# Kernel tuning notes

Hardware: AMD Instinct MI355X
Metric: run time of the kernel (lower is better)

The kernel has to match this reference:

```python
import jax, jax.numpy as jnp
from jax import lax
import numpy as np

DN = ('NCHW', 'OIHW', 'NCHW')

def conv2d_same(x, w, b):
    # 5x5, stride 1, pad 2 == SAME
    y = lax.conv_general_dilated(x, w, (1, 1), 'SAME', dimension_numbers=DN)
    return y + b[None, :, None, None]

def setup_inputs() -> dict:
    key = jax.random.key(0)
    ks = jax.random.split(key, 5)
    B, S, D = 8, 2048, 1024
    k55 = 0.2  # ~1/sqrt(25) init scale
    return {
        'x':  jax.random.normal(ks[0], (B, S, D), dtype=jnp.float32),
        'w1': jax.random.normal(ks[1], (1, 1, 5, 5), dtype=jnp.float32) * k55,
        'b1': jnp.zeros((1,), jnp.float32),
        'w2': jax.random.normal(ks[2], (1, 1, 5, 5), dtype=jnp.float32) * k55,
        'b2': jnp.zeros((1,), jnp.float32),
        'w3': jax.random.normal(ks[3], (1, 2, 5, 5), dtype=jnp.float32) * k55,
        'b3': jnp.zeros((1,), jnp.float32),
        'w4': jax.random.normal(ks[4], (1, 1, 5, 5), dtype=jnp.float32) * k55,
        'b4': jnp.zeros((1,), jnp.float32),
    }

def reference(x, w1, b1, w2, b2, w3, b3, w4, b4):
    # x: [b, s, d]
    xT = jnp.swapaxes(x, 1, 2)                              # [b, d, s]
    # self-similarity, softmax over BATCH dim (dim=0, as in original)
    NSSM = jax.nn.softmax(jnp.einsum('bsd,btd->bst', x, x), axis=0)   # [b, s, s]
    conv_x  = conv2d_same(x[:, None],  w1, b1)[:, 0]        # [b, s, d]
    conv_xT = conv2d_same(xT[:, None], w2, b2)[:, 0]        # [b, d, s]
    Attention_map = jax.nn.softmax(jnp.matmul(conv_x, conv_xT), axis=0)  # [b, s, s]
    Moca_map = conv2d_same(jnp.stack([NSSM, Attention_map], axis=1), w3, b3)[:, 0]  # [b, s, s]
    conv_g = conv2d_same(x[:, None], w4, b4)[:, 0]          # [b, s, d]
    Wz = jnp.matmul(Moca_map, conv_g)                       # [b, s, d]
    return Wz + x
```

## Files before the change

### kernel.cpp

```cpp
#include <hip/hip_runtime.h>

#define Bz 8
#define Sz 2048
#define Dz 1024

typedef __attribute__((ext_vector_type(8))) _Float16 f16x8;
typedef __attribute__((ext_vector_type(8))) short short8v;
typedef __attribute__((ext_vector_type(4))) short short4v;
typedef __attribute__((ext_vector_type(4))) float f32x4;

__device__ __forceinline__ short f2h(float f) {
    _Float16 h = (_Float16)f;
    return __builtin_bit_cast(short, h);
}
__device__ __forceinline__ float h2f(short s) {
    return (float)__builtin_bit_cast(_Float16, s);
}
__device__ __forceinline__ void gld16(const void* g, void* l) {
    __builtin_amdgcn_global_load_lds(
        (const __attribute__((address_space(1))) void*)g,
        (__attribute__((address_space(3))) void*)l, 16, 0, 0);
}

__global__ __launch_bounds__(256) void conv3_kernel(
    const float* __restrict__ x,
    const float* __restrict__ w1, const float* __restrict__ b1,
    const float* __restrict__ w2, const float* __restrict__ b2,
    short* __restrict__ x16, short* __restrict__ C1f, short* __restrict__ C2f)
{
    __shared__ float w[50];
    __shared__ float bias[2];
    const size_t SD = (size_t)Sz * Dz;
    int tid = threadIdx.x;
    if (tid < 25) w[tid] = w1[tid];
    else if (tid < 50) w[tid] = w2[tid - 25];
    if (tid == 50) { bias[0] = b1[0]; bias[1] = b2[0]; }
    __syncthreads();

    int d4 = tid * 4;
    int y = blockIdx.y;
    int s = ((y & 7) << 8) | (y >> 3);
    int b = blockIdx.z;
    const float* xb = x + (size_t)b * SD + d4;

    float wv[5][12];
#pragma unroll
    for (int i = 0; i < 5; i++) {
        int ss = s + i - 2;
        int ssc = ss < 0 ? 0 : (ss >= Sz ? Sz - 1 : ss);
        const float* rp = xb + (size_t)ssc * Dz;
        if (d4 > 0) *(float4*)&wv[i][0] = *(const float4*)(rp - 4);
        else { wv[i][0] = wv[i][1] = wv[i][2] = wv[i][3] = 0.f; }
        *(float4*)&wv[i][4] = *(const float4*)rp;
        if (d4 < 1020) *(float4*)&wv[i][8] = *(const float4*)(rp + 4);
        else { wv[i][8] = wv[i][9] = wv[i][10] = wv[i][11] = 0.f; }
        if (ss != ssc) {
#pragma unroll
            for (int q = 0; q < 12; q++) wv[i][q] = 0.f;
        }
    }

    float o1[4] = {}, o2[4] = {};
#pragma unroll
    for (int i = 0; i < 5; i++)
#pragma unroll
        for (int j = 0; j < 5; j++) {
            float c1w = w[i * 5 + j], c2w = w[25 + j * 5 + i];
#pragma unroll
            for (int q = 0; q < 4; q++) {
                float v = wv[i][q + j + 2];
                o1[q] = fmaf(c1w, v, o1[q]);
                o2[q] = fmaf(c2w, v, o2[q]);
            }
        }
    size_t o = (size_t)b * SD + (size_t)s * Dz + d4;
    short4v hx, h1, h2;
#pragma unroll
    for (int q = 0; q < 4; q++) {
        hx[q] = f2h(wv[2][q + 4]);
        h1[q] = f2h(o1[q] + bias[0]);
        h2[q] = f2h(o2[q] + bias[1]);
    }
    *(short4v*)(x16 + o) = hx;
    *(short4v*)(C1f + o) = h1;
    *(short4v*)(C2f + o) = h2;
}

__global__ __launch_bounds__(256) void convT_kernel(
    const float* __restrict__ x, const float* __restrict__ w4,
    const float* __restrict__ b4, short* __restrict__ C4T)
{
    __shared__ float xs[68][73];
    __shared__ short ct[64][72];
    __shared__ float w[25];
    __shared__ float bb;
    const size_t SD = (size_t)Sz * Dz;
    int tid = threadIdx.x;
    if (tid < 25) w[tid] = w4[tid];
    if (tid == 25) bb = b4[0];

    int s0 = blockIdx.x * 64, d0 = blockIdx.y * 64, b = blockIdx.z;
    const float* xb = x + (size_t)b * SD;
    for (int k = tid; k < 68 * 68; k += 256) {
        int r = k / 68, c = k - r * 68;
        int gr = s0 - 2 + r, gc = d0 - 2 + c;
        float v = 0.f;
        if (gr >= 0 && gr < Sz && gc >= 0 && gc < Dz) v = xb[(size_t)gr * Dz + gc];
        xs[r][c] = v;
    }
    __syncthreads();

    int sl = tid & 63, dg = tid >> 6;
    float acc[16];
#pragma unroll
    for (int q = 0; q < 16; q++) acc[q] = bb;
#pragma unroll
    for (int i = 0; i < 5; i++) {
        float row[20];
#pragma unroll
        for (int m = 0; m < 20; m++) row[m] = xs[sl + i][dg * 16 + m];
#pragma unroll
        for (int j = 0; j < 5; j++) {
            float wv = w[i * 5 + j];
#pragma unroll
            for (int q = 0; q < 16; q++) acc[q] = fmaf(wv, row[q + j], acc[q]);
        }
    }
#pragma unroll
    for (int q = 0; q < 16; q++) ct[dg * 16 + q][sl] = f2h(acc[q]);
    __syncthreads();

    int dl = tid >> 2, sc = (tid & 3) * 16;
    f16x8 v0 = *(const f16x8*)&ct[dl][sc];
    f16x8 v1 = *(const f16x8*)&ct[dl][sc + 8];
    short* op = C4T + (size_t)b * SD + (size_t)(d0 + dl) * Sz + s0 + sc;
    *(f16x8*)op = v0;
    *(f16x8*)(op + 8) = v1;
}

__global__ __launch_bounds__(512) void logit_f16(
    const short* __restrict__ Ag, const short* __restrict__ Bg,
    const short* __restrict__ Aa, const short* __restrict__ Ba,
    short* __restrict__ Qg, short* __restrict__ Qa,
    int rlo, int sqoff, long PS)
{
    __shared__ short sA[3][4096];
    __shared__ short sB[3][4096];

    int flat = blockIdx.x + 16 * (blockIdx.y + 8 * blockIdx.z);
    int nid = (flat & 7) * 256 + (flat >> 3);
    int bx = nid & 15;
    int by = (nid >> 4) & 7;
    int bz = nid >> 7;

    const int map = bz >> 3, bzb = bz & 7;
    if (map == 0) {
        int nt = bx - sqoff;
        if (nt >= 0 && nt < 8 && nt < by) return;
    }

    const size_t SD = (size_t)Sz * Dz;
    const int K = Dz;
    const short* A = (map ? Aa : Ag) + (size_t)bzb * SD;
    const short* B = (map ? Ba : Bg) + (size_t)bzb * SD;
    short* Q = (map ? Qa : Qg) + (size_t)bzb * PS;

    const int m0 = by * 128, n0 = bx * 128;
    const int t = threadIdx.x;
    const int lane = t & 63;
    const int w = t >> 6;
    const int wm = w >> 2, wn = w & 3;
    const int fr = lane & 15;
    const int kb = lane >> 4;

    const int s_  = (t & 7) ^ ((t >> 3) & 7);
    const int h_  = s_ >> 2, kbs = s_ & 3;
    const int lrow = t >> 3;
    const int rowAs = m0 + lrow + h_ * 64;
    const int rowBs = n0 + lrow + h_ * 64;
    const size_t aOff = (size_t)rowAs * K * 2 + kbs * 16;
    const size_t bOff = (size_t)rowBs * K * 2 + kbs * 16;

    int rdA[4], rdB[2];
#pragma unroll
    for (int f = 0; f < 4; f++) {
        int row = wm * 64 + f * 16 + fr;
        rdA[f] = (row & 63) * 128 + ((((row >> 6) * 4 + kb) ^ (fr & 7)) * 16);
    }
#pragma unroll
    for (int g = 0; g < 2; g++) {
        int row = wn * 32 + g * 16 + fr;
        rdB[g] = (row & 63) * 128 + ((((row >> 6) * 4 + kb) ^ (fr & 7)) * 16);
    }

    f32x4 acc[4][2];
#pragma unroll
    for (int i = 0; i < 4; i++)
#pragma unroll
        for (int j = 0; j < 2; j++) acc[i][j] = (f32x4){0.f, 0.f, 0.f, 0.f};

    auto STAGE = [&](int buf, int k0) {
        gld16((const char*)A + aOff + (size_t)k0 * 2, (char*)&sA[buf][0] + t * 16);
        gld16((const char*)B + bOff + (size_t)k0 * 2, (char*)&sB[buf][0] + t * 16);
    };
    auto COMPUTE = [&](int buf) {
        const char* pA = (const char*)&sA[buf][0];
        const char* pB = (const char*)&sB[buf][0];
        f16x8 af[4], bfr[2];
#pragma unroll
        for (int f = 0; f < 4; f++) af[f] = *(const f16x8*)(pA + rdA[f]);
#pragma unroll
        for (int g = 0; g < 2; g++) bfr[g] = *(const f16x8*)(pB + rdB[g]);
#pragma unroll
        for (int mf = 0; mf < 4; mf++)
#pragma unroll
            for (int nf = 0; nf < 2; nf++)
                acc[mf][nf] = __builtin_amdgcn_mfma_f32_16x16x32_f16(af[mf], bfr[nf], acc[mf][nf], 0, 0, 0);
    };

    const int niter = K / 32;
    STAGE(0, 0);
    STAGE(1, 32);
    int cs = 0, ss = 2;
    for (int it = 0; it < niter; ++it) {
        if (it < niter - 1) { asm volatile("s_waitcnt vmcnt(2)" ::: "memory"); }
        else                { asm volatile("s_waitcnt vmcnt(0)" ::: "memory"); }
        __builtin_amdgcn_sched_barrier(0);
        __builtin_amdgcn_s_barrier();
        if (it + 2 < niter) STAGE(ss, (it + 2) * 32);
        COMPUTE(cs);
        cs = cs == 2 ? 0 : cs + 1;
        ss = ss == 2 ? 0 : ss + 1;
    }

#pragma unroll
    for (int mf = 0; mf < 4; mf++)
#pragma unroll
        for (int nf = 0; nf < 2; nf++) {
            int col = n0 + wn * 32 + nf * 16 + fr;
#pragma unroll
            for (int r = 0; r < 4; r++) {
                int rowg = m0 + wm * 64 + mf * 16 + kb * 4 + r;
                float o = acc[mf][nf][r];
                if (map == 0 && rlo + rowg == col) o -= 1024.f;
                Q[(size_t)rowg * Sz + col] = f2h(o);
            }
        }
}

__global__ __launch_bounds__(256) void mirror_g(
    short* __restrict__ F, int o0, long PS)
{
    __shared__ short ts[128][136];
    int p = blockIdx.x, b = blockIdx.y;
    int mi = 1, base = 0;
    while (p >= base + mi) { base += mi; mi++; }
    int nt = p - base;
    short* Fb = F + (size_t)b * PS;
    int t = threadIdx.x;
    int rr = t >> 1, c0 = (t & 1) * 64;
    const short* src = Fb + (size_t)(nt * 128 + rr) * Sz + o0 + mi * 128 + c0;
#pragma unroll
    for (int j = 0; j < 8; j++)
        *(short8v*)&ts[rr][c0 + j * 8] = *(const short8v*)(src + j * 8);
    __syncthreads();
    short* dst = Fb + (size_t)(mi * 128 + rr) * Sz + o0 + nt * 128 + c0;
#pragma unroll
    for (int j = 0; j < 8; j++) {
        short8v v;
#pragma unroll
        for (int e = 0; e < 8; e++) v[e] = ts[c0 + j * 8 + e][rr];
        *(short8v*)(dst + j * 8) = v;
    }
}

__global__ __launch_bounds__(256) void softmax_ip(
    short* __restrict__ Qg, short* __restrict__ Qa, int nElem, long ps)
{
    int i8 = (blockIdx.x * 256 + threadIdx.x) * 8;
    if (i8 >= nElem) return;
    short* Q = blockIdx.z ? Qa : Qg;

    short8v v[Bz];
    float f[Bz][8];
#pragma unroll
    for (int b = 0; b < Bz; b++) {
        v[b] = *(const short8v*)(Q + i8 + (size_t)b * ps);
#pragma unroll
        for (int e = 0; e < 8; e++) f[b][e] = h2f(v[b][e]);
    }
#pragma unroll
    for (int e = 0; e < 8; e++) {
        float mx = f[0][e];
#pragma unroll
        for (int b = 1; b < Bz; b++) mx = fmaxf(mx, f[b][e]);
        float sum = 0.f;
#pragma unroll
        for (int b = 0; b < Bz; b++) { f[b][e] = __expf(f[b][e] - mx); sum += f[b][e]; }
        float inv = 1.f / sum;
#pragma unroll
        for (int b = 0; b < Bz; b++) v[b][e] = f2h(f[b][e] * inv);
    }
#pragma unroll
    for (int b = 0; b < Bz; b++)
        *(short8v*)(Q + i8 + (size_t)b * ps) = v[b];
}

__global__ __launch_bounds__(256) void slab_copy(
    const short* __restrict__ Fg, const short* __restrict__ Fa,
    short* __restrict__ slab, long PS)
{
    int idx = blockIdx.x * 256 + threadIdx.x;
    int e = idx * 8;
    int map = e >> 16;
    int rem = e & 65535;
    int b = rem >> 13;
    int rem2 = rem & 8191;
    int row = rem2 >> 11;
    int col = rem2 & 2047;
    const short* src = (map ? Fa : Fg) + (size_t)b * PS + (size_t)(1020 + row) * Sz + col;
    *(short8v*)(slab + e) = *(const short8v*)src;
}

__global__ __launch_bounds__(256) void moca_kernel(
    const short* __restrict__ Gs, const short* __restrict__ As,
    const short* __restrict__ slab,
    const float* __restrict__ w3, const float* __restrict__ b3,
    short* __restrict__ Mout,
    int o0, int rlo, int slabLo, long psIn, long psOut)
{
    __shared__ float w[50];
    __shared__ float bb;
    int tid = threadIdx.x;
    if (tid < 50) w[tid] = w3[tid];
    if (tid == 50) bb = b3[0];
    __syncthreads();

    int t8 = tid * 8;
    int so = blockIdx.y, b = blockIdx.z;
    int s = o0 + so;
    const short* Gp = Gs + (size_t)b * psIn;
    const short* Ap = As + (size_t)b * psIn;

    float acc[8];
#pragma unroll
    for (int q = 0; q < 8; q++) acc[q] = bb;

#pragma unroll
    for (int i = 0; i < 5; i++) {
        int sr = s + i - 2;
        if (sr < 0 || sr >= Sz) continue;
        const short *gp, *ap;
        size_t ro;
        if (sr >= rlo) { gp = Gp; ap = Ap; ro = (size_t)(sr - rlo) * Sz; }
        else {
            gp = slab + (size_t)b * 8192;
            ap = slab + 65536 + (size_t)b * 8192;
            ro = (size_t)(sr - slabLo) * Sz;
        }
        float gw[16], aw[16];
#pragma unroll
        for (int g = 0; g < 4; g++) {
            int c0 = t8 - 4 + g * 4;
            if (c0 >= 0 && c0 + 3 < Sz) {
                short4v gv = *(const short4v*)(gp + ro + c0);
                short4v av = *(const short4v*)(ap + ro + c0);
#pragma unroll
                for (int e = 0; e < 4; e++) { gw[g * 4 + e] = h2f(gv[e]); aw[g * 4 + e] = h2f(av[e]); }
            } else {
#pragma unroll
                for (int e = 0; e < 4; e++) { gw[g * 4 + e] = 0.f; aw[g * 4 + e] = 0.f; }
            }
        }
#pragma unroll
        for (int j = 0; j < 5; j++) {
            float wg = w[i * 5 + j], wa = w[25 + i * 5 + j];
#pragma unroll
            for (int q = 0; q < 8; q++)
                acc[q] = fmaf(wg, gw[q + j + 2], fmaf(wa, aw[q + j + 2], acc[q]));
        }
    }
    short4v r0, r1;
#pragma unroll
    for (int q = 0; q < 4; q++) { r0[q] = f2h(acc[q]); r1[q] = f2h(acc[q + 4]); }
    short* op = Mout + (size_t)b * psOut + (size_t)so * Sz + t8;
    *(short4v*)op = r0;
    *(short4v*)(op + 4) = r1;
}

__global__ __launch_bounds__(512) void gemm_wz(
    const short* __restrict__ A, const short* __restrict__ B,
    const float* __restrict__ Src, float* __restrict__ C,
    int M, long sAb)
{
    __shared__ short sA[3][4096];
    __shared__ short sB[3][4096];

    int gx = gridDim.x, gy = gridDim.y;
    int total = gx * gy * gridDim.z;
    int flat = blockIdx.x + gx * (blockIdx.y + gy * blockIdx.z);
    int cpx = total >> 3;
    int nid = (flat & 7) * cpx + (flat >> 3);
    int bx = nid % gx;
    int tmp = nid / gx;
    int by = tmp % gy;
    int bz = tmp / gy;

    const size_t SD = (size_t)Sz * Dz;
    const int K = Sz;
    A += (size_t)bz * sAb;
    B += (size_t)bz * SD;
    Src += (size_t)bz * SD;
    C += (size_t)bz * SD;

    const int m0 = by * 128, n0 = bx * 128;
    const int t = threadIdx.x;
    const int lane = t & 63;
    const int w = t >> 6;
    const int wm = w >> 2, wn = w & 3;
    const int fr = lane & 15;
    const int kb = lane >> 4;

    const int s_  = (t & 7) ^ ((t >> 3) & 7);
    const int h_  = s_ >> 2, kbs = s_ & 3;
    const int lrow = t >> 3;
    int rowAs = m0 + lrow + h_ * 64; if (rowAs > M - 1) rowAs = M - 1;
    const int rowBs = n0 + lrow + h_ * 64;
    const size_t aOff = (size_t)rowAs * K * 2 + kbs * 16;
    const size_t bOff = (size_t)rowBs * K * 2 + kbs * 16;

    int rdA[4], rdB[2];
#pragma unroll
    for (int f = 0; f < 4; f++) {
        int row = wm * 64 + f * 16 + fr;
        rdA[f] = (row & 63) * 128 + ((((row >> 6) * 4 + kb) ^ (fr & 7)) * 16);
    }
#pragma unroll
    for (int g = 0; g < 2; g++) {
        int row = wn * 32 + g * 16 + fr;
        rdB[g] = (row & 63) * 128 + ((((row >> 6) * 4 + kb) ^ (fr & 7)) * 16);
    }

    f32x4 acc[4][2];
#pragma unroll
    for (int i = 0; i < 4; i++)
#pragma unroll
        for (int j = 0; j < 2; j++) acc[i][j] = (f32x4){0.f, 0.f, 0.f, 0.f};

    auto STAGE = [&](int buf, int k0) {
        gld16((const char*)A + aOff + (size_t)k0 * 2, (char*)&sA[buf][0] + t * 16);
        gld16((const char*)B + bOff + (size_t)k0 * 2, (char*)&sB[buf][0] + t * 16);
    };
    auto COMPUTE = [&](int buf) {
        const char* pA = (const char*)&sA[buf][0];
        const char* pB = (const char*)&sB[buf][0];
        f16x8 af[4], bfr[2];
#pragma unroll
        for (int f = 0; f < 4; f++) af[f] = *(const f16x8*)(pA + rdA[f]);
#pragma unroll
        for (int g = 0; g < 2; g++) bfr[g] = *(const f16x8*)(pB + rdB[g]);
#pragma unroll
        for (int mf = 0; mf < 4; mf++)
#pragma unroll
            for (int nf = 0; nf < 2; nf++)
                acc[mf][nf] = __builtin_amdgcn_mfma_f32_16x16x32_f16(af[mf], bfr[nf], acc[mf][nf], 0, 0, 0);
    };

    const int niter = K / 32;
    STAGE(0, 0);
    STAGE(1, 32);
    int cs = 0, ss = 2;
    for (int it = 0; it < niter; ++it) {
        if (it < niter - 1) { asm volatile("s_waitcnt vmcnt(2)" ::: "memory"); }
        else                { asm volatile("s_waitcnt vmcnt(0)" ::: "memory"); }
        __builtin_amdgcn_sched_barrier(0);
        __builtin_amdgcn_s_barrier();
        if (it + 2 < niter) STAGE(ss, (it + 2) * 32);
        COMPUTE(cs);
        cs = cs == 2 ? 0 : cs + 1;
        ss = ss == 2 ? 0 : ss + 1;
    }

#pragma unroll
    for (int mf = 0; mf < 4; mf++)
#pragma unroll
        for (int nf = 0; nf < 2; nf++) {
            int col = n0 + wn * 32 + nf * 16 + fr;
#pragma unroll
            for (int r = 0; r < 4; r++) {
                int rowg = m0 + wm * 64 + mf * 16 + kb * 4 + r;
                if (rowg < M)
                    C[(size_t)rowg * Dz + col] = acc[mf][nf][r] + Src[(size_t)rowg * Dz + col];
            }
        }
}

extern "C" void kernel_launch(void* const* d_in, const int* in_sizes, int n_in,
                              void* d_out, int out_size, void* d_ws, size_t ws_size,
                              hipStream_t stream)
{
    const float* x  = (const float*)d_in[0];
    const float* w1 = (const float*)d_in[1];
    const float* b1 = (const float*)d_in[2];
    const float* w2 = (const float*)d_in[3];
    const float* b2 = (const float*)d_in[4];
    const float* w3 = (const float*)d_in[5];
    const float* b3 = (const float*)d_in[6];
    const float* w4 = (const float*)d_in[7];
    const float* b4 = (const float*)d_in[8];
    float* out = (float*)d_out;

    const size_t SD = (size_t)Sz * Dz;
    const size_t BSD2 = (size_t)Bz * SD * 2;

    char* ws = (char*)d_ws;
    short* x16 = (short*)(ws);
    short* C1f = (short*)(ws + 1 * BSD2);
    short* C2f = (short*)(ws + 2 * BSD2);
    short* C4T = (short*)(ws + 3 * BSD2);
    char* strip0 = ws + 4 * BSD2;

    const size_t PS  = (size_t)1024 * Sz;
    const size_t PSM = (size_t)1026 * Sz;
    short* Fg   = (short*)strip0;
    short* Fa   = Fg + (size_t)Bz * PS;
    short* Mf   = Fa + (size_t)Bz * PS;
    short* slab = Mf + (size_t)Bz * PSM;

    conv3_kernel<<<dim3(1, Sz, Bz), 256, 0, stream>>>(
        x, w1, b1, w2, b2, x16, C1f, C2f);
    convT_kernel<<<dim3(Sz / 64, Dz / 64, Bz), 256, 0, stream>>>(x, w4, b4, C4T);

    const int ne = 1024 * Sz;

    logit_f16<<<dim3(16, 8, 16), 512, 0, stream>>>(
        x16, x16, C1f, C2f, Fg, Fa, 0, 0, (long)PS);
    mirror_g<<<dim3(28, Bz), 256, 0, stream>>>(Fg, 0, (long)PS);
    softmax_ip<<<dim3((ne / 8 + 255) / 256, 1, 2), 256, 0, stream>>>(Fg, Fa, ne, (long)PS);
    slab_copy<<<dim3(64), 256, 0, stream>>>(Fg, Fa, slab, (long)PS);
    moca_kernel<<<dim3(1, 1022, Bz), 256, 0, stream>>>(
        Fg, Fa, slab, w3, b3, Mf, 0, 0, 0, (long)PS, (long)PSM);
    gemm_wz<<<dim3(Dz / 128, 8, Bz), 512, 0, stream>>>(
        Mf, C4T, x, out, 1022, (long)PSM);

    logit_f16<<<dim3(16, 8, 16), 512, 0, stream>>>(
        x16 + (size_t)1024 * Dz, x16, C1f + (size_t)1024 * Dz, C2f,
        Fg, Fa, 1024, 8, (long)PS);
    mirror_g<<<dim3(28, Bz), 256, 0, stream>>>(Fg, 1024, (long)PS);
    softmax_ip<<<dim3((ne / 8 + 255) / 256, 1, 2), 256, 0, stream>>>(Fg, Fa, ne, (long)PS);
    moca_kernel<<<dim3(1, 1026, Bz), 256, 0, stream>>>(
        Fg, Fa, slab, w3, b3, Mf, 1022, 1024, 1020, (long)PS, (long)PSM);
    gemm_wz<<<dim3(Dz / 128, 9, Bz), 512, 0, stream>>>(
        Mf, C4T, x + (size_t)1022 * Dz, out + (size_t)1022 * Dz, 1026, (long)PSM);
}
```

Measured before the change: 628.8 us.

## Enlarge logit GEMM tiles to 256x256 with a double-buffered quarter-step MFMA schedule

Replaces the 128x128 logit GEMM with a 256x256-tile kernel. It uses a 128KB LDS double buffer over 64-wide K tiles and issues MFMAs in four quadrant phases per K half. Loads are interleaved with barriers and vmcnt waits, and s_setprio raises priority around the MFMA bursts. The goal is higher arithmetic intensity and less global/LDS traffic per FLOP in the dominant logit matmuls. The cost is coarser symmetry skipping at 256-tile granularity, so some redundant diagonal work is done, and only one block fits per CU.

```diff
diff --git a/kernel.cpp b/kernel.cpp
--- a/kernel.cpp
+++ b/kernel.cpp
@@ -138,25 +138,21 @@
     *(f16x8*)(op + 8) = v1;
 }
 
-__global__ __launch_bounds__(512) void logit_f16(
+__global__ __launch_bounds__(512, 2) void logit8_f16(
     const short* __restrict__ Ag, const short* __restrict__ Bg,
     const short* __restrict__ Aa, const short* __restrict__ Ba,
     short* __restrict__ Qg, short* __restrict__ Qa,
-    int rlo, int sqoff, long PS)
-{
-    __shared__ short sA[3][4096];
-    __shared__ short sB[3][4096];
-
-    int flat = blockIdx.x + 16 * (blockIdx.y + 8 * blockIdx.z);
-    int nid = (flat & 7) * 256 + (flat >> 3);
-    int bx = nid & 15;
-    int by = (nid >> 4) & 7;
-    int bz = nid >> 7;
-
+    int rlo, int sq256off, long PS)
+{
+    __shared__ char lds[131072];
+
+    int flat = blockIdx.x + 8 * (blockIdx.y + 4 * blockIdx.z);
+    int nid = (flat & 7) * 64 + (flat >> 3);
+    int bx = nid & 7, by = (nid >> 3) & 3, bz = nid >> 5;
     const int map = bz >> 3, bzb = bz & 7;
     if (map == 0) {
-        int nt = bx - sqoff;
-        if (nt >= 0 && nt < 8 && nt < by) return;
+        int ntl = bx - sq256off;
+        if (ntl >= 0 && ntl < 4 && ntl < by) return;
     }
 
     const size_t SD = (size_t)Sz * Dz;
@@ -164,6 +160,310 @@
     const short* A = (map ? Aa : Ag) + (size_t)bzb * SD;
     const short* B = (map ? Ba : Bg) + (size_t)bzb * SD;
     short* Q = (map ? Qa : Qg) + (size_t)bzb * PS;
+
+    const int m0 = by * 256, n0 = bx * 256;
+    const int t = threadIdx.x;
+    const int lane = t & 63;
+    const int w = t >> 6;
+    const int wm = w >> 2, wn = w & 3;
+    const int fr = lane & 15;
+    const int kb = lane >> 4;
+
+    const int cc16 = ((t & 7) ^ ((t >> 3) & 7)) * 16;
+    const int tr = t >> 3;
+    const int bdst = (t >> 8) * 8192 + ((t >> 3) & 31) * 128 + (t & 7) * 16;
+
+    auto STA = [&](int tile, int h) {
+        char* base = lds + (tile & 1) * 65536;
+#pragma unroll
+        for (int j = 0; j < 2; j++) {
+            int row = m0 + j * 128 + h * 64 + tr;
+            gld16((const char*)A + ((size_t)row * K + tile * 64) * 2 + cc16,
+                  base + j * 16384 + h * 8192 + t * 16);
+        }
+    };
+    auto STB = [&](int tile, int h) {
+        char* base = lds + (tile & 1) * 65536 + 32768;
+#pragma unroll
+        for (int j = 0; j < 2; j++) {
+            int u = j * 64 + tr;
+            int row = n0 + (u >> 5) * 64 + h * 32 + (u & 31);
+            gld16((const char*)B + ((size_t)row * K + tile * 64) * 2 + cc16,
+                  base + j * 16384 + h * 4096 + bdst);
+        }
+    };
+
+    int aoff[2], boff[2];
+#pragma unroll
+    for (int ks = 0; ks < 2; ks++) {
+        int slot = ((ks * 4 + kb) ^ (fr & 7)) * 16;
+        aoff[ks] = (wm * 128 + fr) * 128 + slot;
+        boff[ks] = (wn * 64 + fr) * 128 + slot;
+    }
+
+    f16x8 aR[8];
+    f16x8 bR[2][4];
+    f32x4 acc[8][4];
+#pragma unroll
+    for (int i = 0; i < 8; i++)
+#pragma unroll
+        for (int j = 0; j < 4; j++) acc[i][j] = (f32x4){0.f, 0.f, 0.f, 0.f};
+
+    auto LDA = [&](int qa, int d) {
+        const char* p = lds + d * 65536 + qa * 8192;
+#pragma unroll
+        for (int f = 0; f < 4; f++)
+#pragma unroll
+            for (int ks = 0; ks < 2; ks++)
+                aR[f * 2 + ks] = *(const f16x8*)(p + aoff[ks] + f * 2048);
+    };
+    auto LDB = [&](int qb, int d, int which) {
+        const char* p = lds + d * 65536 + 32768 + qb * 4096;
+#pragma unroll
+        for (int g = 0; g < 2; g++)
+#pragma unroll
+            for (int ks = 0; ks < 2; ks++)
+                bR[which][g * 2 + ks] = *(const f16x8*)(p + boff[ks] + g * 2048);
+    };
+#define MMQ(qa, qb, which)                                                        \
+    __builtin_amdgcn_s_setprio(1);                                                \
+    _Pragma("unroll") for (int f = 0; f < 4; f++)                                 \
+        _Pragma("unroll") for (int g = 0; g < 2; g++)                             \
+            _Pragma("unroll") for (int ks = 0; ks < 2; ks++)                      \
+                acc[(qa)*4 + f][(qb)*2 + g] = __builtin_amdgcn_mfma_f32_16x16x32_f16( \
+                    aR[f * 2 + ks], bR[which][g * 2 + ks], acc[(qa)*4 + f][(qb)*2 + g], 0, 0, 0); \
+    __builtin_amdgcn_s_setprio(0);
+
+#define BAR()  __builtin_amdgcn_s_barrier(); __builtin_amdgcn_sched_barrier(0)
+#define WAIT4() asm volatile("s_waitcnt vmcnt(4)" ::: "memory"); __builtin_amdgcn_sched_barrier(0)
+#define WAIT0() asm volatile("s_waitcnt vmcnt(0)" ::: "memory"); __builtin_amdgcn_sched_barrier(0)
+
+    STA(0, 0); STB(0, 0); STA(0, 1); STB(0, 1);
+    STA(1, 0); STB(1, 0);
+
+    const int NIT = K / 128;
+    for (int it = 0; it < NIT - 1; ++it) {
+        const int V = 2 * it + 1, W = 2 * it + 2, X = 2 * it + 3;
+        WAIT4(); BAR();
+        STA(V, 1); LDA(0, 0); LDB(0, 0, 0); MMQ(0, 0, 0);
+        BAR();
+        STB(V, 1); LDB(1, 0, 1); MMQ(0, 1, 1);
+        BAR();
+        STA(W, 0); LDA(1, 0); MMQ(1, 0, 0);
+        BAR();
+        STB(W, 0); MMQ(1, 1, 1);
+        WAIT4(); BAR();
+        STA(W, 1); LDA(0, 1); LDB(0, 1, 0); MMQ(0, 0, 0);
+        BAR();
+        STB(W, 1); LDB(1, 1, 1); MMQ(0, 1, 1);
+        BAR();
+        STA(X, 0); LDA(1, 1); MMQ(1, 0, 0);
+        BAR();
+        STB(X, 0); MMQ(1, 1, 1);
+    }
+    {
+        const int V = 2 * NIT - 1;
+        WAIT4(); BAR();
+        STA(V, 1); LDA(0, 0); LDB(0, 0, 0); MMQ(0, 0, 0);
+        BAR();
+        STB(V, 1); LDB(1, 0, 1); MMQ(0, 1, 1);
+        BAR();
+        LDA(1, 0); MMQ(1, 0, 0);
+        BAR();
+        MMQ(1, 1, 1);
+        WAIT0(); BAR();
+        LDA(0, 1); LDB(0, 1, 0); MMQ(0, 0, 0);
+        BAR();
+        LDB(1, 1, 1); MMQ(0, 1, 1);
+        BAR();
+        LDA(1, 1); MMQ(1, 0, 0);
+        BAR();
+        MMQ(1, 1, 1);
+    }
+#undef MMQ
+#undef BAR
+#undef WAIT4
+#undef WAIT0
+
+#pragma unroll
+    for (int mf = 0; mf < 8; mf++)
+#pragma unroll
+        for (int nf = 0; nf < 4; nf++) {
+            int col = n0 + wn * 64 + nf * 16 + fr;
+#pragma unroll
+            for (int r = 0; r < 4; r++) {
+                int rowg = m0 + wm * 128 + mf * 16 + kb * 4 + r;
+                float o = acc[mf][nf][r];
+                if (map == 0 && rlo + rowg == col) o -= 1024.f;
+                Q[(size_t)rowg * Sz + col] = f2h(o);
+            }
+        }
+}
+
+__global__ __launch_bounds__(256) void mirror_g(
+    short* __restrict__ F, int o0, long PS)
+{
+    __shared__ short ts[128][136];
+    int p = blockIdx.x, b = blockIdx.y;
+    int mi = 1, base = 0;
+    while (p >= base + mi) { base += mi; mi++; }
+    int nt = p - base;
+    short* Fb = F + (size_t)b * PS;
+    int t = threadIdx.x;
+    int rr = t >> 1, c0 = (t & 1) * 64;
+    const short* src = Fb + (size_t)(nt * 128 + rr) * Sz + o0 + mi * 128 + c0;
+#pragma unroll
+    for (int j = 0; j < 8; j++)
+        *(short8v*)&ts[rr][c0 + j * 8] = *(const short8v*)(src + j * 8);
+    __syncthreads();
+    short* dst = Fb + (size_t)(mi * 128 + rr) * Sz + o0 + nt * 128 + c0;
+#pragma unroll
+    for (int j = 0; j < 8; j++) {
+        short8v v;
+#pragma unroll
+        for (int e = 0; e < 8; e++) v[e] = ts[c0 + j * 8 + e][rr];
+        *(short8v*)(dst + j * 8) = v;
+    }
+}
+
+__global__ __launch_bounds__(256) void softmax_ip(
+    short* __restrict__ Qg, short* __restrict__ Qa, int nElem, long ps)
+{
+    int i8 = (blockIdx.x * 256 + threadIdx.x) * 8;
+    if (i8 >= nElem) return;
+    short* Q = blockIdx.z ? Qa : Qg;
+
+    short8v v[Bz];
+    float f[Bz][8];
+#pragma unroll
+    for (int b = 0; b < Bz; b++) {
+        v[b] = *(const short8v*)(Q + i8 + (size_t)b * ps);
+#pragma unroll
+        for (int e = 0; e < 8; e++) f[b][e] = h2f(v[b][e]);
+    }
+#pragma unroll
+    for (int e = 0; e < 8; e++) {
+        float mx = f[0][e];
+#pragma unroll
+        for (int b = 1; b < Bz; b++) mx = fmaxf(mx, f[b][e]);
+        float sum = 0.f;
+#pragma unroll
+        for (int b = 0; b < Bz; b++) { f[b][e] = __expf(f[b][e] - mx); sum += f[b][e]; }
+        float inv = 1.f / sum;
+#pragma unroll
+        for (int b = 0; b < Bz; b++) v[b][e] = f2h(f[b][e] * inv);
+    }
+#pragma unroll
+    for (int b = 0; b < Bz; b++)
+        *(short8v*)(Q + i8 + (size_t)b * ps) = v[b];
+}
+
+__global__ __launch_bounds__(256) void slab_copy(
+    const short* __restrict__ Fg, const short* __restrict__ Fa,
+    short* __restrict__ slab, long PS)
+{
+    int idx = blockIdx.x * 256 + threadIdx.x;
+    int e = idx * 8;
+    int map = e >> 16;
+    int rem = e & 65535;
+    int b = rem >> 13;
+    int rem2 = rem & 8191;
+    int row = rem2 >> 11;
+    int col = rem2 & 2047;
+    const short* src = (map ? Fa : Fg) + (size_t)b * PS + (size_t)(1020 + row) * Sz + col;
+    *(short8v*)(slab + e) = *(const short8v*)src;
+}
+
+__global__ __launch_bounds__(256) void moca_kernel(
+    const short* __restrict__ Gs, const short* __restrict__ As,
+    const short* __restrict__ slab,
+    const float* __restrict__ w3, const float* __restrict__ b3,
+    short* __restrict__ Mout,
+    int o0, int rlo, int slabLo, long psIn, long psOut)
+{
+    __shared__ float w[50];
+    __shared__ float bb;
+    int tid = threadIdx.x;
+    if (tid < 50) w[tid] = w3[tid];
+    if (tid == 50) bb = b3[0];
+    __syncthreads();
+
+    int t8 = tid * 8;
+    int so = blockIdx.y, b = blockIdx.z;
+    int s = o0 + so;
+    const short* Gp = Gs + (size_t)b * psIn;
+    const short* Ap = As + (size_t)b * psIn;
+
+    float acc[8];
+#pragma unroll
+    for (int q = 0; q < 8; q++) acc[q] = bb;
+
+#pragma unroll
+    for (int i = 0; i < 5; i++) {
+        int sr = s + i - 2;
+        if (sr < 0 || sr >= Sz) continue;
+        const short *gp, *ap;
+        size_t ro;
+        if (sr >= rlo) { gp = Gp; ap = Ap; ro = (size_t)(sr - rlo) * Sz; }
+        else {
+            gp = slab + (size_t)b * 8192;
+            ap = slab + 65536 + (size_t)b * 8192;
+            ro = (size_t)(sr - slabLo) * Sz;
+        }
+        float gw[16], aw[16];
+#pragma unroll
+        for (int g = 0; g < 4; g++) {
+            int c0 = t8 - 4 + g * 4;
+            if (c0 >= 0 && c0 + 3 < Sz) {
+                short4v gv = *(const short4v*)(gp + ro + c0);
+                short4v av = *(const short4v*)(ap + ro + c0);
+#pragma unroll
+                for (int e = 0; e < 4; e++) { gw[g * 4 + e] = h2f(gv[e]); aw[g * 4 + e] = h2f(av[e]); }
+            } else {
+#pragma unroll
+                for (int e = 0; e < 4; e++) { gw[g * 4 + e] = 0.f; aw[g * 4 + e] = 0.f; }
+            }
+        }
+#pragma unroll
+        for (int j = 0; j < 5; j++) {
+            float wg = w[i * 5 + j], wa = w[25 + i * 5 + j];
+#pragma unroll
+            for (int q = 0; q < 8; q++)
+                acc[q] = fmaf(wg, gw[q + j + 2], fmaf(wa, aw[q + j + 2], acc[q]));
+        }
+    }
+    short4v r0, r1;
+#pragma unroll
+    for (int q = 0; q < 4; q++) { r0[q] = f2h(acc[q]); r1[q] = f2h(acc[q + 4]); }
+    short* op = Mout + (size_t)b * psOut + (size_t)so * Sz + t8;
+    *(short4v*)op = r0;
+    *(short4v*)(op + 4) = r1;
+}
+
+__global__ __launch_bounds__(512) void gemm_wz(
+    const short* __restrict__ A, const short* __restrict__ B,
+    const float* __restrict__ Src, float* __restrict__ C,
+    int M, long sAb)
+{
+    __shared__ short sA[3][4096];
+    __shared__ short sB[3][4096];
+
+    int gx = gridDim.x, gy = gridDim.y;
+    int total = gx * gy * gridDim.z;
+    int flat = blockIdx.x + gx * (blockIdx.y + gy * blockIdx.z);
+    int cpx = total >> 3;
+    int nid = (flat & 7) * cpx + (flat >> 3);
+    int bx = nid % gx;
+    int tmp = nid / gx;
+    int by = tmp % gy;
+    int bz = tmp / gy;
+
+    const size_t SD = (size_t)Sz * Dz;
+    const int K = Sz;
+    A += (size_t)bz * sAb;
+    B += (size_t)bz * SD;
+    Src += (size_t)bz * SD;
+    C += (size_t)bz * SD;
 
     const int m0 = by * 128, n0 = bx * 128;
     const int t = threadIdx.x;
@@ -176,7 +476,7 @@
     const int s_  = (t & 7) ^ ((t >> 3) & 7);
     const int h_  = s_ >> 2, kbs = s_ & 3;
     const int lrow = t >> 3;
-    const int rowAs = m0 + lrow + h_ * 64;
+    int rowAs = m0 + lrow + h_ * 64; if (rowAs > M - 1) rowAs = M - 1;
     const int rowBs = n0 + lrow + h_ * 64;
     const size_t aOff = (size_t)rowAs * K * 2 + kbs * 16;
     const size_t bOff = (size_t)rowBs * K * 2 + kbs * 16;
@@ -241,254 +541,6 @@
 #pragma unroll
             for (int r = 0; r < 4; r++) {
                 int rowg = m0 + wm * 64 + mf * 16 + kb * 4 + r;
-                float o = acc[mf][nf][r];
-                if (map == 0 && rlo + rowg == col) o -= 1024.f;
-                Q[(size_t)rowg * Sz + col] = f2h(o);
-            }
-        }
-}
-
-__global__ __launch_bounds__(256) void mirror_g(
-    short* __restrict__ F, int o0, long PS)
-{
-    __shared__ short ts[128][136];
-    int p = blockIdx.x, b = blockIdx.y;
-    int mi = 1, base = 0;
-    while (p >= base + mi) { base += mi; mi++; }
-    int nt = p - base;
-    short* Fb = F + (size_t)b * PS;
-    int t = threadIdx.x;
-    int rr = t >> 1, c0 = (t & 1) * 64;
-    const short* src = Fb + (size_t)(nt * 128 + rr) * Sz + o0 + mi * 128 + c0;
-#pragma unroll
-    for (int j = 0; j < 8; j++)
-        *(short8v*)&ts[rr][c0 + j * 8] = *(const short8v*)(src + j * 8);
-    __syncthreads();
-    short* dst = Fb + (size_t)(mi * 128 + rr) * Sz + o0 + nt * 128 + c0;
-#pragma unroll
-    for (int j = 0; j < 8; j++) {
-        short8v v;
-#pragma unroll
-        for (int e = 0; e < 8; e++) v[e] = ts[c0 + j * 8 + e][rr];
-        *(short8v*)(dst + j * 8) = v;
-    }
-}
-
-__global__ __launch_bounds__(256) void softmax_ip(
-    short* __restrict__ Qg, short* __restrict__ Qa, int nElem, long ps)
-{
-    int i8 = (blockIdx.x * 256 + threadIdx.x) * 8;
-    if (i8 >= nElem) return;
-    short* Q = blockIdx.z ? Qa : Qg;
-
-    short8v v[Bz];
-    float f[Bz][8];
-#pragma unroll
-    for (int b = 0; b < Bz; b++) {
-        v[b] = *(const short8v*)(Q + i8 + (size_t)b * ps);
-#pragma unroll
-        for (int e = 0; e < 8; e++) f[b][e] = h2f(v[b][e]);
-    }
-#pragma unroll
-    for (int e = 0; e < 8; e++) {
-        float mx = f[0][e];
-#pragma unroll
-        for (int b = 1; b < Bz; b++) mx = fmaxf(mx, f[b][e]);
-        float sum = 0.f;
-#pragma unroll
-        for (int b = 0; b < Bz; b++) { f[b][e] = __expf(f[b][e] - mx); sum += f[b][e]; }
-        float inv = 1.f / sum;
-#pragma unroll
-        for (int b = 0; b < Bz; b++) v[b][e] = f2h(f[b][e] * inv);
-    }
-#pragma unroll
-    for (int b = 0; b < Bz; b++)
-        *(short8v*)(Q + i8 + (size_t)b * ps) = v[b];
-}
-
-__global__ __launch_bounds__(256) void slab_copy(
-    const short* __restrict__ Fg, const short* __restrict__ Fa,
-    short* __restrict__ slab, long PS)
-{
-    int idx = blockIdx.x * 256 + threadIdx.x;
-    int e = idx * 8;
-    int map = e >> 16;
-    int rem = e & 65535;
-    int b = rem >> 13;
-    int rem2 = rem & 8191;
-    int row = rem2 >> 11;
-    int col = rem2 & 2047;
-    const short* src = (map ? Fa : Fg) + (size_t)b * PS + (size_t)(1020 + row) * Sz + col;
-    *(short8v*)(slab + e) = *(const short8v*)src;
-}
-
-__global__ __launch_bounds__(256) void moca_kernel(
-    const short* __restrict__ Gs, const short* __restrict__ As,
-    const short* __restrict__ slab,
-    const float* __restrict__ w3, const float* __restrict__ b3,
-    short* __restrict__ Mout,
-    int o0, int rlo, int slabLo, long psIn, long psOut)
-{
-    __shared__ float w[50];
-    __shared__ float bb;
-    int tid = threadIdx.x;
-    if (tid < 50) w[tid] = w3[tid];
-    if (tid == 50) bb = b3[0];
-    __syncthreads();
-
-    int t8 = tid * 8;
-    int so = blockIdx.y, b = blockIdx.z;
-    int s = o0 + so;
-    const short* Gp = Gs + (size_t)b * psIn;
-    const short* Ap = As + (size_t)b * psIn;
-
-    float acc[8];
-#pragma unroll
-    for (int q = 0; q < 8; q++) acc[q] = bb;
-
-#pragma unroll
-    for (int i = 0; i < 5; i++) {
-        int sr = s + i - 2;
-        if (sr < 0 || sr >= Sz) continue;
-        const short *gp, *ap;
-        size_t ro;
-        if (sr >= rlo) { gp = Gp; ap = Ap; ro = (size_t)(sr - rlo) * Sz; }
-        else {
-            gp = slab + (size_t)b * 8192;
-            ap = slab + 65536 + (size_t)b * 8192;
-            ro = (size_t)(sr - slabLo) * Sz;
-        }
-        float gw[16], aw[16];
-#pragma unroll
-        for (int g = 0; g < 4; g++) {
-            int c0 = t8 - 4 + g * 4;
-            if (c0 >= 0 && c0 + 3 < Sz) {
-                short4v gv = *(const short4v*)(gp + ro + c0);
-                short4v av = *(const short4v*)(ap + ro + c0);
-#pragma unroll
-                for (int e = 0; e < 4; e++) { gw[g * 4 + e] = h2f(gv[e]); aw[g * 4 + e] = h2f(av[e]); }
-            } else {
-#pragma unroll
-                for (int e = 0; e < 4; e++) { gw[g * 4 + e] = 0.f; aw[g * 4 + e] = 0.f; }
-            }
-        }
-#pragma unroll
-        for (int j = 0; j < 5; j++) {
-            float wg = w[i * 5 + j], wa = w[25 + i * 5 + j];
-#pragma unroll
-            for (int q = 0; q < 8; q++)
-                acc[q] = fmaf(wg, gw[q + j + 2], fmaf(wa, aw[q + j + 2], acc[q]));
-        }
-    }
-    short4v r0, r1;
-#pragma unroll
-    for (int q = 0; q < 4; q++) { r0[q] = f2h(acc[q]); r1[q] = f2h(acc[q + 4]); }
-    short* op = Mout + (size_t)b * psOut + (size_t)so * Sz + t8;
-    *(short4v*)op = r0;
-    *(short4v*)(op + 4) = r1;
-}
-
-__global__ __launch_bounds__(512) void gemm_wz(
-    const short* __restrict__ A, const short* __restrict__ B,
-    const float* __restrict__ Src, float* __restrict__ C,
-    int M, long sAb)
-{
-    __shared__ short sA[3][4096];
-    __shared__ short sB[3][4096];
-
-    int gx = gridDim.x, gy = gridDim.y;
-    int total = gx * gy * gridDim.z;
-    int flat = blockIdx.x + gx * (blockIdx.y + gy * blockIdx.z);
-    int cpx = total >> 3;
-    int nid = (flat & 7) * cpx + (flat >> 3);
-    int bx = nid % gx;
-    int tmp = nid / gx;
-    int by = tmp % gy;
-    int bz = tmp / gy;
-
-    const size_t SD = (size_t)Sz * Dz;
-    const int K = Sz;
-    A += (size_t)bz * sAb;
-    B += (size_t)bz * SD;
-    Src += (size_t)bz * SD;
-    C += (size_t)bz * SD;
-
-    const int m0 = by * 128, n0 = bx * 128;
-    const int t = threadIdx.x;
-    const int lane = t & 63;
-    const int w = t >> 6;
-    const int wm = w >> 2, wn = w & 3;
-    const int fr = lane & 15;
-    const int kb = lane >> 4;
-
-    const int s_  = (t & 7) ^ ((t >> 3) & 7);
-    const int h_  = s_ >> 2, kbs = s_ & 3;
-    const int lrow = t >> 3;
-    int rowAs = m0 + lrow + h_ * 64; if (rowAs > M - 1) rowAs = M - 1;
-    const int rowBs = n0 + lrow + h_ * 64;
-    const size_t aOff = (size_t)rowAs * K * 2 + kbs * 16;
-    const size_t bOff = (size_t)rowBs * K * 2 + kbs * 16;
-
-    int rdA[4], rdB[2];
-#pragma unroll
-    for (int f = 0; f < 4; f++) {
-        int row = wm * 64 + f * 16 + fr;
-        rdA[f] = (row & 63) * 128 + ((((row >> 6) * 4 + kb) ^ (fr & 7)) * 16);
-    }
-#pragma unroll
-    for (int g = 0; g < 2; g++) {
-        int row = wn * 32 + g * 16 + fr;
-        rdB[g] = (row & 63) * 128 + ((((row >> 6) * 4 + kb) ^ (fr & 7)) * 16);
-    }
-
-    f32x4 acc[4][2];
-#pragma unroll
-    for (int i = 0; i < 4; i++)
-#pragma unroll
-        for (int j = 0; j < 2; j++) acc[i][j] = (f32x4){0.f, 0.f, 0.f, 0.f};
-
-    auto STAGE = [&](int buf, int k0) {
-        gld16((const char*)A + aOff + (size_t)k0 * 2, (char*)&sA[buf][0] + t * 16);
-        gld16((const char*)B + bOff + (size_t)k0 * 2, (char*)&sB[buf][0] + t * 16);
-    };
-    auto COMPUTE = [&](int buf) {
-        const char* pA = (const char*)&sA[buf][0];
-        const char* pB = (const char*)&sB[buf][0];
-        f16x8 af[4], bfr[2];
-#pragma unroll
-        for (int f = 0; f < 4; f++) af[f] = *(const f16x8*)(pA + rdA[f]);
-#pragma unroll
-        for (int g = 0; g < 2; g++) bfr[g] = *(const f16x8*)(pB + rdB[g]);
-#pragma unroll
-        for (int mf = 0; mf < 4; mf++)
-#pragma unroll
-            for (int nf = 0; nf < 2; nf++)
-                acc[mf][nf] = __builtin_amdgcn_mfma_f32_16x16x32_f16(af[mf], bfr[nf], acc[mf][nf], 0, 0, 0);
-    };
-
-    const int niter = K / 32;
-    STAGE(0, 0);
-    STAGE(1, 32);
-    int cs = 0, ss = 2;
-    for (int it = 0; it < niter; ++it) {
-        if (it < niter - 1) { asm volatile("s_waitcnt vmcnt(2)" ::: "memory"); }
-        else                { asm volatile("s_waitcnt vmcnt(0)" ::: "memory"); }
-        __builtin_amdgcn_sched_barrier(0);
-        __builtin_amdgcn_s_barrier();
-        if (it + 2 < niter) STAGE(ss, (it + 2) * 32);
-        COMPUTE(cs);
-        cs = cs == 2 ? 0 : cs + 1;
-        ss = ss == 2 ? 0 : ss + 1;
-    }
-
-#pragma unroll
-    for (int mf = 0; mf < 4; mf++)
-#pragma unroll
-        for (int nf = 0; nf < 2; nf++) {
-            int col = n0 + wn * 32 + nf * 16 + fr;
-#pragma unroll
-            for (int r = 0; r < 4; r++) {
-                int rowg = m0 + wm * 64 + mf * 16 + kb * 4 + r;
                 if (rowg < M)
                     C[(size_t)rowg * Dz + col] = acc[mf][nf][r] + Src[(size_t)rowg * Dz + col];
             }
@@ -533,7 +585,7 @@
 
     const int ne = 1024 * Sz;
 
-    logit_f16<<<dim3(16, 8, 16), 512, 0, stream>>>(
+    logit8_f16<<<dim3(8, 4, 16), 512, 0, stream>>>(
         x16, x16, C1f, C2f, Fg, Fa, 0, 0, (long)PS);
     mirror_g<<<dim3(28, Bz), 256, 0, stream>>>(Fg, 0, (long)PS);
     softmax_ip<<<dim3((ne / 8 + 255) / 256, 1, 2), 256, 0, stream>>>(Fg, Fa, ne, (long)PS);
@@ -543,9 +595,9 @@
     gemm_wz<<<dim3(Dz / 128, 8, Bz), 512, 0, stream>>>(
         Mf, C4T, x, out, 1022, (long)PSM);
 
-    logit_f16<<<dim3(16, 8, 16), 512, 0, stream>>>(
+    logit8_f16<<<dim3(8, 4, 16), 512, 0, stream>>>(
         x16 + (size_t)1024 * Dz, x16, C1f + (size_t)1024 * Dz, C2f,
-        Fg, Fa, 1024, 8, (long)PS);
+        Fg, Fa, 1024, 4, (long)PS);
     mirror_g<<<dim3(28, Bz), 256, 0, stream>>>(Fg, 1024, (long)PS);
     softmax_ip<<<dim3((ne / 8 + 255) / 256, 1, 2), 256, 0, stream>>>(Fg, Fa, ne, (long)PS);
     moca_kernel<<<dim3(1, 1026, Bz), 256, 0, stream>>>(
```

Result: faster. 572.0 us (-9.0%).
